# Kernel optimization log

Hardware: AMD Instinct MI355X
Metric: run time of the kernel (lower is better)

Reference implementation:

```python
import jax, jax.numpy as jnp
import numpy as np

B, T, E, H = 2, 2048, 1024, 16
D = E // H
K_KEEP = 391
RECENCY = 64
SCALE = D ** -0.5


def setup_inputs() -> dict:
    key = jax.random.key(0)
    k1, k2, k3 = jax.random.split(key, 3)
    x = jax.random.normal(k1, (B, T, E), jnp.float32)
    W_attn = jax.random.normal(k2, (3 * E, E), jnp.float32) * 0.02  # torch Linear weight [out,in]
    W_proj = jax.random.normal(k3, (E, E), jnp.float32) * 0.02
    return {"x": x, "W_attn": W_attn, "W_proj": W_proj}


def reference(x, W_attn, W_proj):
    b, t, c = x.shape
    qkv = x @ W_attn.T                      # [B,T,3E]
    q, k, v = jnp.split(qkv, 3, axis=-1)
    to_heads = lambda u: u.reshape(b, t, H, D).transpose(0, 2, 1, 3)  # [B,H,T,D]
    q, k, v = to_heads(q), to_heads(k), to_heads(v)

    # first pass: causal attention weights for importance scoring
    scores = jnp.einsum('bhqd,bhkd->bhqk', q, k) * SCALE
    causal = jnp.tril(jnp.ones((t, t), dtype=bool))
    scores = jnp.where(causal, scores, -jnp.inf)
    attn_w = jax.nn.softmax(scores, axis=-1)

    # mean importance over query dim, force-keep recent tokens
    imp = attn_w.mean(axis=2)               # [B,H,T]
    imp = imp.at[:, :, -RECENCY:].set(1.0)

    # top-k token selection per (batch, head)
    _, idx = jax.lax.top_k(imp, K_KEEP)     # [B,H,K]

    # gather pruned K/V
    K_keep = jnp.take_along_axis(k, idx[..., None], axis=2)  # [B,H,K,D]
    V_keep = jnp.take_along_axis(v, idx[..., None], axis=2)

    # second attention pass over pruned keys (no causal mask, matches legacy code)
    s2 = jnp.einsum('bhqd,bhkd->bhqk', q, K_keep) * SCALE
    a2 = jax.nn.softmax(s2, axis=-1)
    out = jnp.einsum('bhqk,bhkd->bhqd', a2, V_keep)          # [B,H,T,D]

    out = out.transpose(0, 2, 1, 3).reshape(b, t, c)
    return out @ W_proj.T
```

## Files before the change

kernel.cpp:

```cpp
#include <hip/hip_runtime.h>
#include <hip/hip_bf16.h>


#define TT 2048
#define EE 1024
#define HH 16
#define DD 64
#define KKEEP 391
#define REC 64
#define NBH 32
#define QSCALE 0.125f
#define KPAD 448

typedef short bf16x8 __attribute__((ext_vector_type(8)));
typedef _Float16 f16x8 __attribute__((ext_vector_type(8)));
typedef float f32x4 __attribute__((ext_vector_type(4)));

#define WAIT_VM(N) asm volatile("s_waitcnt vmcnt(" #N ")" ::: "memory")
#define WAIT_LGKM0 asm volatile("s_waitcnt lgkmcnt(0)" ::: "memory")
#define BAR() __builtin_amdgcn_s_barrier()

static __device__ inline unsigned short bf_rn(float x) {
  unsigned u = __float_as_uint(x);
  unsigned r = u + 0x7fffu + ((u >> 16) & 1u);
  return (unsigned short)(r >> 16);
}
static __device__ inline float bf_up(unsigned short h) {
  return __uint_as_float((unsigned)h << 16);
}
static __device__ inline unsigned pkf16(float a, float b) {
  union { _Float16 h[2]; unsigned u; } t;
  t.h[0] = (_Float16)a; t.h[1] = (_Float16)b; return t.u;
}
static __device__ inline void glds16(const void* g, void* l) {
  __builtin_amdgcn_global_load_lds(
      (const __attribute__((address_space(1))) void*)g,
      (__attribute__((address_space(3))) void*)l, 16, 0, 0);
}

static __device__ inline void split4(const float* __restrict__ src,
                                     unsigned short* __restrict__ ho,
                                     unsigned short* __restrict__ lo_, int i)
{
  float4 v = *reinterpret_cast<const float4*>(&src[i]);
  ushort4 hh, ll;
  float f;
  hh.x = bf_rn(v.x); f = bf_up(hh.x); ll.x = bf_rn(v.x - f);
  hh.y = bf_rn(v.y); f = bf_up(hh.y); ll.y = bf_rn(v.y - f);
  hh.z = bf_rn(v.z); f = bf_up(hh.z); ll.z = bf_rn(v.z - f);
  hh.w = bf_rn(v.w); f = bf_up(hh.w); ll.w = bf_rn(v.w - f);
  *reinterpret_cast<ushort4*>(&ho[i]) = hh;
  *reinterpret_cast<ushort4*>(&lo_[i]) = ll;
}

__global__ __launch_bounds__(256) void split_kernel(
    const float* __restrict__ src, unsigned short* __restrict__ ho,
    unsigned short* __restrict__ lo_, int n)
{
  int i = (blockIdx.x * 256 + threadIdx.x) * 4;
  const int stride = gridDim.x * 1024;
  for (; i < n; i += stride) split4(src, ho, lo_, i);
}

__global__ __launch_bounds__(256) void split2_kernel(
    const float* __restrict__ x, const float* __restrict__ wa,
    unsigned short* __restrict__ xh, unsigned short* __restrict__ xl,
    unsigned short* __restrict__ wh, unsigned short* __restrict__ wl)
{
  const int n1 = 4096 * 1024, n2 = 3072 * 1024;
  int i = (blockIdx.x * 256 + threadIdx.x) * 4;
  const int stride = gridDim.x * 1024;
  for (; i < n1 + n2; i += stride) {
    if (i < n1) split4(x, xh, xl, i);
    else        split4(wa, wh, wl, i - n1);
  }
}

__global__ __launch_bounds__(256) void add_kernel(
    const float* __restrict__ p0, const float* __restrict__ p1,
    float* __restrict__ out, int n)
{
  int i = (blockIdx.x * 256 + threadIdx.x) * 4;
  const int stride = gridDim.x * 1024;
  for (; i < n; i += stride) {
    float4 a = *reinterpret_cast<const float4*>(&p0[i]);
    float4 b = *reinterpret_cast<const float4*>(&p1[i]);
    *reinterpret_cast<float4*>(&out[i]) =
        make_float4(a.x + b.x, a.y + b.y, a.z + b.z, a.w + b.w);
  }
}

template<bool VB, int MODE>
__global__ __launch_bounds__(256) void gemm_pipe(
    const unsigned short* __restrict__ Ah, const unsigned short* __restrict__ Al,
    const unsigned short* __restrict__ Bh, const unsigned short* __restrict__ Bl,
    float* __restrict__ Cc, unsigned short* __restrict__ Qho, unsigned short* __restrict__ Qlo,
    unsigned short* __restrict__ Kho, unsigned short* __restrict__ Klo,
    float* __restrict__ Vo, int M, int N, int Kd, int ldAB, int nOff)
{
  __shared__ __align__(16) unsigned short Ahs[2][128 * 32];
  __shared__ __align__(16) unsigned short Bhs[2][128 * 32];
  __shared__ __align__(16) unsigned short Als[VB ? 1 : 2][128 * 32];
  __shared__ __align__(16) unsigned short Bls[VB ? 1 : 2][128 * 32];
  const int tid = threadIdx.x;
  const int m0 = blockIdx.y * 128, n0 = nOff + blockIdx.x * 128;
  const int kOff = blockIdx.z * Kd;
  const int w = tid >> 6, lane = tid & 63;
  const int wm = w >> 1, wn = w & 1;
  const int l15 = lane & 15, l4 = lane >> 4;

  size_t gA[2], gB[2]; int ldso[2];
#pragma unroll
  for (int s = 0; s < 2; s++) {
    int seg = w * 2 + s;
    int r = seg * 16 + (lane >> 2);
    int kb = (lane & 3) ^ ((r >> 1) & 3);
    gA[s] = (size_t)(m0 + r) * ldAB + kOff + kb * 8;
    gB[s] = (size_t)(n0 + r) * ldAB + kOff + kb * 8;
    ldso[s] = seg * 512;
  }
  auto STAGE = [&](int bb, int k0) {
#pragma unroll
    for (int s = 0; s < 2; s++) {
      glds16(&Ah[gA[s] + k0], &Ahs[bb][ldso[s]]);
      glds16(&Bh[gB[s] + k0], &Bhs[bb][ldso[s]]);
      if (!VB) {
        glds16(&Al[gA[s] + k0], &Als[bb][ldso[s]]);
        glds16(&Bl[gB[s] + k0], &Bls[bb][ldso[s]]);
      }
    }
  };

  f32x4 acc[4][4] = {};

  STAGE(0, 0);
  STAGE(1, 32);
  int cur = 0;
  for (int k0 = 0; k0 < Kd; k0 += 32) {
    if (k0 + 32 < Kd) { if (VB) WAIT_VM(4); else WAIT_VM(8); }
    else WAIT_VM(0);
    BAR();
    bf16x8 ah[4], al[4], bh[4], bl[4];
#pragma unroll
    for (int i = 0; i < 4; i++) {
      int ar = wm * 64 + i * 16 + l15;
      int aoff = ar * 32 + ((l4 ^ ((ar >> 1) & 3)) * 8);
      ah[i] = *reinterpret_cast<const bf16x8*>(&Ahs[cur][aoff]);
      int br = wn * 64 + i * 16 + l15;
      int boff = br * 32 + ((l4 ^ ((br >> 1) & 3)) * 8);
      bh[i] = *reinterpret_cast<const bf16x8*>(&Bhs[cur][boff]);
      if (!VB) {
        al[i] = *reinterpret_cast<const bf16x8*>(&Als[cur][aoff]);
        bl[i] = *reinterpret_cast<const bf16x8*>(&Bls[cur][boff]);
      }
    }
#pragma unroll
    for (int i = 0; i < 4; i++)
#pragma unroll
      for (int j = 0; j < 4; j++) {
        acc[i][j] = __builtin_amdgcn_mfma_f32_16x16x32_bf16(ah[i], bh[j], acc[i][j], 0, 0, 0);
        if (!VB) {
          acc[i][j] = __builtin_amdgcn_mfma_f32_16x16x32_bf16(ah[i], bl[j], acc[i][j], 0, 0, 0);
          acc[i][j] = __builtin_amdgcn_mfma_f32_16x16x32_bf16(al[i], bh[j], acc[i][j], 0, 0, 0);
        }
      }
    WAIT_LGKM0;
    BAR();
    if (k0 + 64 < Kd) STAGE(cur, k0 + 64);
    cur ^= 1;
  }

  if (MODE == 0) {
    float* Cout = Cc + (size_t)blockIdx.z * ((size_t)M * N);
#pragma unroll
    for (int i = 0; i < 4; i++) {
      int mrow0 = m0 + wm * 64 + i * 16 + l4 * 4;
#pragma unroll
      for (int j = 0; j < 4; j++) {
        int ncol = n0 + wn * 64 + j * 16 + l15;
#pragma unroll
        for (int r = 0; r < 4; r++)
          Cout[(size_t)(mrow0 + r) * N + ncol] = acc[i][j][r];
      }
    }
  } else if (VB) {
#pragma unroll
    for (int j = 0; j < 4; j++) {
      int n = n0 + wn * 64 + j * 16 + l15;
      int rr = n & 1023;
      int h = rr >> 6, d0 = rr & 63;
#pragma unroll
      for (int i = 0; i < 4; i++) {
        int mrow0 = m0 + wm * 64 + i * 16 + l4 * 4;
#pragma unroll
        for (int r = 0; r < 4; r++) {
          int m = mrow0 + r;
          int b = m >> 11, t = m & 2047;
          Vo[((size_t)((b * HH + h) * TT + t)) * DD + d0] = acc[i][j][r];
        }
      }
    }
  } else {
#pragma unroll
    for (int j = 0; j < 4; j++) {
      int n = n0 + wn * 64 + j * 16 + l15;
      int p = n >> 10, rr = n & 1023;
      int h = rr >> 6, d0 = rr & 63;
#pragma unroll
      for (int i = 0; i < 4; i++) {
        int mrow0 = m0 + wm * 64 + i * 16 + l4 * 4;
#pragma unroll
        for (int r = 0; r < 4; r++) {
          int m = mrow0 + r;
          int b = m >> 11, t = m & 2047;
          size_t idx = ((size_t)((b * HH + h) * TT + t)) * DD + d0;
          float v = acc[i][j][r];
          unsigned short hi_ = bf_rn(v);
          unsigned short lo2 = bf_rn(v - bf_up(hi_));
          if (p == 0) { Qho[idx] = hi_; Qlo[idx] = lo2; }
          else        { Kho[idx] = hi_; Klo[idx] = lo2; }
        }
      }
    }
  }
}

__global__ __launch_bounds__(512, 4) void importance6_kernel(
    const unsigned short* __restrict__ Qh, const unsigned short* __restrict__ Ql,
    const unsigned short* __restrict__ Kh, const unsigned short* __restrict__ Kl,
    float* __restrict__ part)
{
  const int bh = blockIdx.x;
  const int y = (int)blockIdx.y;
  const int rt = (y < 8) ? (15 - y) : (y - 8);
  const int slab = y;
  const int row0 = rt * 128;
  const int nch = 2 * rt + 2;
  const int tid = threadIdx.x;
  const int w = tid >> 6, lane = tid & 63;
  const int wm = w >> 1, wn = w & 1;
  const int l15 = lane & 15, l4 = lane >> 4;
  __shared__ __align__(16) unsigned short Khs[2][64 * 64];
  __shared__ __align__(16) unsigned short Kls[2][64 * 64];
  __shared__ float csw[8 * 32];
  __shared__ float rsb[2 * 128];

  const int kr = w * 8 + (lane >> 3);
  const int sk8 = (lane & 7) ^ (kr & 7);
  const int ldw = w * 512;
  auto STAGEK1 = [&](int bb, int ci) {
    glds16(&Kh[((size_t)(bh * TT + ci * 64 + kr)) * DD + sk8 * 8], &Khs[bb][ldw]);
  };
  auto STAGEK2 = [&](int bb, int ci) {
    size_t ga = ((size_t)(bh * TT + ci * 64 + kr)) * DD + sk8 * 8;
    glds16(&Kh[ga], &Khs[bb][ldw]);
    glds16(&Kl[ga], &Kls[bb][ldw]);
  };

  bf16x8 aq[2][2];
#pragma unroll
  for (int ks = 0; ks < 2; ks++)
#pragma unroll
    for (int i = 0; i < 2; i++) {
      int ar = wm * 32 + i * 16 + l15;
      size_t ga = ((size_t)(bh * TT + row0 + ar)) * DD + (ks * 4 + l4) * 8;
      aq[ks][i] = *reinterpret_cast<const bf16x8*>(&Qh[ga]);
    }

  float rsum[2][4];
#pragma unroll
  for (int i = 0; i < 2; i++)
#pragma unroll
    for (int r = 0; r < 4; r++) rsum[i][r] = 0.f;

  STAGEK1(0, 0);
  STAGEK1(1, 1);
  int cur = 0;
  for (int ci = 0; ci < nch; ci++) {
    if (ci + 1 < nch) WAIT_VM(1); else WAIT_VM(0);
    BAR();
    f32x4 acc[2][2] = {};
#pragma unroll
    for (int ks = 0; ks < 2; ks++) {
#pragma unroll
      for (int j = 0; j < 2; j++) {
        int br = wn * 32 + j * 16 + l15;
        int off = br * 64 + (((ks * 4 + l4) ^ (br & 7)) * 8);
        bf16x8 bh_ = *reinterpret_cast<const bf16x8*>(&Khs[cur][off]);
#pragma unroll
        for (int i = 0; i < 2; i++)
          acc[i][j] = __builtin_amdgcn_mfma_f32_16x16x32_bf16(aq[ks][i], bh_, acc[i][j], 0, 0, 0);
      }
    }
    if (ci >= 2 * rt) {
#pragma unroll
      for (int i = 0; i < 2; i++)
#pragma unroll
        for (int r = 0; r < 4; r++) {
          int row = row0 + wm * 32 + i * 16 + l4 * 4 + r;
          float s = 0.f;
#pragma unroll
          for (int j = 0; j < 2; j++) {
            int key = ci * 64 + wn * 32 + j * 16 + l15;
            float p = __expf(acc[i][j][r] * QSCALE);
            if (key > row) p = 0.f;
            s += p;
          }
          rsum[i][r] += s;
        }
    } else {
#pragma unroll
      for (int i = 0; i < 2; i++)
#pragma unroll
        for (int r = 0; r < 4; r++) {
          float s = 0.f;
#pragma unroll
          for (int j = 0; j < 2; j++) s += __expf(acc[i][j][r] * QSCALE);
          rsum[i][r] += s;
        }
    }
    WAIT_LGKM0;
    BAR();
    if (ci + 2 < nch) STAGEK1(cur, ci + 2);
    cur ^= 1;
  }
#pragma unroll
  for (int i = 0; i < 2; i++)
#pragma unroll
    for (int r = 0; r < 4; r++) {
      float v = rsum[i][r];
      v += __shfl_xor(v, 1); v += __shfl_xor(v, 2);
      v += __shfl_xor(v, 4); v += __shfl_xor(v, 8);
      rsum[i][r] = v;
    }
  __syncthreads();
  if (l15 == 0) {
#pragma unroll
    for (int i = 0; i < 2; i++)
#pragma unroll
      for (int r = 0; r < 4; r++)
        rsb[wn * 128 + wm * 32 + i * 16 + l4 * 4 + r] = rsum[i][r];
  }
  __syncthreads();
#pragma unroll
  for (int i = 0; i < 2; i++)
#pragma unroll
    for (int r = 0; r < 4; r++) {
      int rl = wm * 32 + i * 16 + l4 * 4 + r;
      rsum[i][r] = 1.0f / (rsb[rl] + rsb[128 + rl]);
    }

  bf16x8 aql[2][2];
#pragma unroll
  for (int ks = 0; ks < 2; ks++)
#pragma unroll
    for (int i = 0; i < 2; i++) {
      int ar = wm * 32 + i * 16 + l15;
      size_t ga = ((size_t)(bh * TT + row0 + ar)) * DD + (ks * 4 + l4) * 8;
      aql[ks][i] = *reinterpret_cast<const bf16x8*>(&Ql[ga]);
    }

  STAGEK2(0, 0);
  STAGEK2(1, 1);
  cur = 0;
  for (int ci = 0; ci < nch; ci++) {
    if (ci + 1 < nch) WAIT_VM(2); else WAIT_VM(0);
    BAR();
    f32x4 acc[2][2] = {};
#pragma unroll
    for (int ks = 0; ks < 2; ks++) {
#pragma unroll
      for (int j = 0; j < 2; j++) {
        int br = wn * 32 + j * 16 + l15;
        int off = br * 64 + (((ks * 4 + l4) ^ (br & 7)) * 8);
        bf16x8 bh_ = *reinterpret_cast<const bf16x8*>(&Khs[cur][off]);
        bf16x8 bl_ = *reinterpret_cast<const bf16x8*>(&Kls[cur][off]);
#pragma unroll
        for (int i = 0; i < 2; i++) {
          acc[i][j] = __builtin_amdgcn_mfma_f32_16x16x32_bf16(aq[ks][i], bh_, acc[i][j], 0, 0, 0);
          acc[i][j] = __builtin_amdgcn_mfma_f32_16x16x32_bf16(aq[ks][i], bl_, acc[i][j], 0, 0, 0);
          acc[i][j] = __builtin_amdgcn_mfma_f32_16x16x32_bf16(aql[ks][i], bh_, acc[i][j], 0, 0, 0);
        }
      }
    }
    float cp[2] = {0.f, 0.f};
    if (ci >= 2 * rt) {
#pragma unroll
      for (int i = 0; i < 2; i++)
#pragma unroll
        for (int r = 0; r < 4; r++) {
          int row = row0 + wm * 32 + i * 16 + l4 * 4 + r;
          float il = rsum[i][r];
#pragma unroll
          for (int j = 0; j < 2; j++) {
            int key = ci * 64 + wn * 32 + j * 16 + l15;
            float p = __expf(acc[i][j][r] * QSCALE) * il;
            if (key > row) p = 0.f;
            cp[j] += p;
          }
        }
    } else {
#pragma unroll
      for (int i = 0; i < 2; i++)
#pragma unroll
        for (int r = 0; r < 4; r++) {
          float il = rsum[i][r];
#pragma unroll
          for (int j = 0; j < 2; j++)
            cp[j] += __expf(acc[i][j][r] * QSCALE) * il;
        }
    }
#pragma unroll
    for (int j = 0; j < 2; j++) {
      float v = cp[j];
      v += __shfl_xor(v, 16); v += __shfl_xor(v, 32);
      cp[j] = v;
    }
    WAIT_LGKM0;
    BAR();
    if (ci + 2 < nch) STAGEK2(cur, ci + 2);
    if (l4 == 0) {
#pragma unroll
      for (int j = 0; j < 2; j++)
        csw[w * 32 + j * 16 + l15] = cp[j];
    }
    WAIT_LGKM0;
    BAR();
    if (tid < 64) {
      int wnc = tid >> 5, cl = tid & 31;
      float s = csw[(0 * 2 + wnc) * 32 + cl] + csw[(1 * 2 + wnc) * 32 + cl] +
                csw[(2 * 2 + wnc) * 32 + cl] + csw[(3 * 2 + wnc) * 32 + cl];
      part[((size_t)(bh * 16 + slab)) * 2048 + ci * 64 + tid] = s;
    }
    cur ^= 1;
  }
}

__global__ __launch_bounds__(256) void topk_gather_kernel(
    const float* __restrict__ part,
    const unsigned short* __restrict__ Kh, const unsigned short* __restrict__ Kl,
    const float* __restrict__ V,
    unsigned short* __restrict__ Kf, unsigned short* __restrict__ Vt)
{
  const int bh = blockIdx.x, tid = threadIdx.x;
  const int lane = tid & 63, w = tid >> 6;
  __shared__ int redi[4];
  __shared__ int stot;
  __shared__ int base[256];
  __shared__ int idxb[KKEEP];
  unsigned u[8];
#pragma unroll
  for (int k = 0; k < 8; k++) {
    int e = tid * 8 + k;
    float s = 0.f;
#pragma unroll
    for (int p = 0; p < 16; p++) {
      int rtp = (p < 8) ? (15 - p) : (p - 8);
      if (e < (rtp + 1) * 128) s += part[((size_t)(bh * 16 + p)) * 2048 + e];
    }
    float v = (e >= TT - REC) ? 3.0e3f : s;
    u[k] = __float_as_uint(v);
  }
  unsigned lo = 0u, hi = 0x7f800000u;
  for (int it = 0; it < 31; it++) {
    unsigned mid = lo + ((hi - lo + 1) >> 1);
    int c = 0;
#pragma unroll
    for (int k = 0; k < 8; k++) c += (u[k] >= mid) ? 1 : 0;
#pragma unroll
    for (int off = 1; off <= 32; off <<= 1) c += __shfl_xor(c, off);
    if (lane == 0) redi[w] = c;
    __syncthreads();
    int tot = redi[0] + redi[1] + redi[2] + redi[3];
    if (tot >= KKEEP) lo = mid; else hi = mid - 1;
    __syncthreads();
  }
  const unsigned vstar = lo;
  int cgt = 0, ceq = 0;
#pragma unroll
  for (int k = 0; k < 8; k++) { cgt += (u[k] > vstar) ? 1 : 0; ceq += (u[k] == vstar) ? 1 : 0; }
  base[tid] = cgt; __syncthreads();
  if (tid == 0) {
    int run = 0;
    for (int i = 0; i < 256; i++) { int t = base[i]; base[i] = run; run += t; }
    stot = run;
  }
  __syncthreads();
  int off1 = base[tid];
#pragma unroll
  for (int k = 0; k < 8; k++)
    if (u[k] > vstar) idxb[off1++] = tid * 8 + k;
  __syncthreads();
  base[tid] = ceq; __syncthreads();
  if (tid == 0) {
    int run = 0;
    for (int i = 0; i < 256; i++) { int t = base[i]; base[i] = run; run += t; }
  }
  __syncthreads();
  int off2 = stot + base[tid];
#pragma unroll
  for (int k = 0; k < 8; k++)
    if (u[k] == vstar) { if (off2 < KKEEP) idxb[off2] = tid * 8 + k; off2++; }
  __syncthreads();
  for (int f = tid; f < KPAD * 8; f += 256) {
    int kk = f >> 3, c8 = f & 7;
    union { _Float16 h[8]; uint4 v; } o;
#pragma unroll
    for (int j = 0; j < 8; j++) o.h[j] = (_Float16)0.f;
    if (kk < KKEEP) {
      int sr = idxb[kk];
      bf16x8 hv = *reinterpret_cast<const bf16x8*>(&Kh[((size_t)(bh * TT + sr)) * DD + c8 * 8]);
      bf16x8 lv = *reinterpret_cast<const bf16x8*>(&Kl[((size_t)(bh * TT + sr)) * DD + c8 * 8]);
#pragma unroll
      for (int j = 0; j < 8; j++)
        o.h[j] = (_Float16)(bf_up((unsigned short)hv[j]) + bf_up((unsigned short)lv[j]));
    }
    *reinterpret_cast<uint4*>(&Kf[((size_t)(bh * KPAD) + kk) * DD + c8 * 8]) = o.v;
  }
  for (int f = tid; f < KPAD * 8; f += 256) {
    int kk = f >> 3, d8 = f & 7;
    float vv[8];
#pragma unroll
    for (int j = 0; j < 8; j++) vv[j] = 0.f;
    if (kk < KKEEP) {
      int sr = idxb[kk];
      float4 a = *reinterpret_cast<const float4*>(&V[((size_t)(bh * TT + sr)) * DD + d8 * 8]);
      float4 b = *reinterpret_cast<const float4*>(&V[((size_t)(bh * TT + sr)) * DD + d8 * 8 + 4]);
      vv[0] = a.x; vv[1] = a.y; vv[2] = a.z; vv[3] = a.w;
      vv[4] = b.x; vv[5] = b.y; vv[6] = b.z; vv[7] = b.w;
    }
#pragma unroll
    for (int j = 0; j < 8; j++) {
      union { _Float16 h; unsigned short s; } t;
      t.h = (_Float16)vv[j];
      Vt[((size_t)(bh * DD) + d8 * 8 + j) * KPAD + kk] = t.s;
    }
  }
}

__global__ __launch_bounds__(256) void attn4_kernel(
    const unsigned short* __restrict__ Qh, const unsigned short* __restrict__ Ql,
    const unsigned short* __restrict__ Kf, const unsigned short* __restrict__ Vt,
    unsigned short* __restrict__ AOh, unsigned short* __restrict__ AOl)
{
  const int rt = blockIdx.y, bh = blockIdx.x;
  const int tid = threadIdx.x;
  const int w = tid >> 6, lane = tid & 63;
  const int l15 = lane & 15, l4 = lane >> 4;
  __shared__ __align__(16) unsigned short Qs[64 * 64];
  __shared__ __align__(16) unsigned short Ks[2][64 * 64];
  __shared__ __align__(16) unsigned short Vs[2][64 * 64];
  __shared__ float LDSo[4][64][16];
  const int row0 = rt * 64;

  int srow[2], skb[2], slds[2];
#pragma unroll
  for (int s = 0; s < 2; s++) {
    int seg = w * 2 + s;
    int r = seg * 8 + (lane >> 3);
    int k8 = lane & 7;
    srow[s] = r; skb[s] = k8 ^ (r & 7); slds[s] = seg * 512;
  }
  auto STAGEA = [&](int bb, int ci) {
#pragma unroll
    for (int s = 0; s < 2; s++) {
      glds16(&Kf[((size_t)(bh * KPAD) + ci * 64 + srow[s]) * DD + skb[s] * 8], &Ks[bb][slds[s]]);
      glds16(&Vt[((size_t)(bh * DD) + srow[s]) * KPAD + ci * 64 + skb[s] * 8], &Vs[bb][slds[s]]);
    }
  };

#pragma unroll
  for (int it = 0; it < 2; it++) {
    int idx = it * 256 + tid;
    int r = idx >> 3, k8 = idx & 7;
    size_t ga = ((size_t)(bh * TT + row0 + r)) * DD + k8 * 8;
    bf16x8 hv = *reinterpret_cast<const bf16x8*>(&Qh[ga]);
    bf16x8 lv = *reinterpret_cast<const bf16x8*>(&Ql[ga]);
    union { _Float16 h[8]; uint4 v; } q16;
#pragma unroll
    for (int j = 0; j < 8; j++)
      q16.h[j] = (_Float16)(bf_up((unsigned short)hv[j]) + bf_up((unsigned short)lv[j]));
    *reinterpret_cast<uint4*>(&Qs[r * 64 + ((k8 ^ (r & 7)) * 8)]) = q16.v;
  }
  STAGEA(0, 0);
  STAGEA(1, 1);
  WAIT_LGKM0;
  BAR();
  f16x8 bq[2];
#pragma unroll
  for (int ks = 0; ks < 2; ks++) {
    int br = w * 16 + l15;
    bq[ks] = *reinterpret_cast<const f16x8*>(&Qs[br * 64 + (((ks * 4 + l4) ^ (br & 7)) * 8)]);
  }

  f32x4 acc_o[4] = {};
  float rsum = 0.f;
  int cur = 0;

  for (int ci = 0; ci < 7; ci++) {
    if (ci + 1 < 7) WAIT_VM(4); else WAIT_VM(0);
    BAR();
    f32x4 accs[4] = {};
#pragma unroll
    for (int ks = 0; ks < 2; ks++) {
#pragma unroll
      for (int i = 0; i < 4; i++) {
        int kr = i * 16 + l15;
        f16x8 af = *reinterpret_cast<const f16x8*>(&Ks[cur][kr * 64 + (((ks * 4 + l4) ^ (kr & 7)) * 8)]);
        accs[i] = __builtin_amdgcn_mfma_f32_16x16x32_f16(af, bq[ks], accs[i], 0, 0, 0);
      }
    }
    float p[4][4];
#pragma unroll
    for (int i = 0; i < 4; i++)
#pragma unroll
      for (int r = 0; r < 4; r++) {
        int gk = ci * 64 + i * 16 + l4 * 4 + r;
        float pp = __expf(accs[i][r] * QSCALE);
        if (gk >= KKEEP) pp = 0.f;
        p[i][r] = pp;
        rsum += pp;
      }
    unsigned pkU[4][2];
#pragma unroll
    for (int i = 0; i < 4; i++) {
      pkU[i][0] = pkf16(p[i][0], p[i][1]);
      pkU[i][1] = pkf16(p[i][2], p[i][3]);
    }
#pragma unroll
    for (int ks = 0; ks < 2; ks++) {
      union { f16x8 h; unsigned u[4]; } bp;
#pragma unroll
      for (int wp = 0; wp < 4; wp++) {
        int src = ((l4 & 1) * 2 + (wp >> 1)) * 16 + l15;
        unsigned v0 = (unsigned)__shfl((int)pkU[ks * 2][wp & 1], src);
        unsigned v1 = (unsigned)__shfl((int)pkU[ks * 2 + 1][wp & 1], src);
        bp.u[wp] = (l4 & 2) ? v1 : v0;
      }
#pragma unroll
      for (int i = 0; i < 4; i++) {
        int dr = i * 16 + l15;
        f16x8 av = *reinterpret_cast<const f16x8*>(&Vs[cur][dr * 64 + (((ks * 4 + l4) ^ (dr & 7)) * 8)]);
        acc_o[i] = __builtin_amdgcn_mfma_f32_16x16x32_f16(av, bp.h, acc_o[i], 0, 0, 0);
      }
    }
    WAIT_LGKM0;
    BAR();
    if (ci + 2 < 7) STAGEA(cur, ci + 2);
    cur ^= 1;
  }
  rsum += __shfl_xor(rsum, 16);
  rsum += __shfl_xor(rsum, 32);
  float inv = 1.0f / rsum;
#pragma unroll
  for (int i = 0; i < 4; i++)
#pragma unroll
    for (int r = 0; r < 4; r++)
      LDSo[w][i * 16 + l4 * 4 + r][l15] = acc_o[i][r] * inv;
  __syncthreads();
  const int b = bh >> 4, h = bh & 15;
#pragma unroll
  for (int uu = 0; uu < 2; uu++) {
    int u = uu * 64 + lane;
    int q = u >> 3, dc = u & 7;
    int row = row0 + w * 16 + q;
    union { unsigned short s[8]; uint4 v; } sh, sl;
#pragma unroll
    for (int j = 0; j < 8; j++) {
      float v = LDSo[w][dc * 8 + j][q];
      unsigned short hh = bf_rn(v);
      sh.s[j] = hh;
      sl.s[j] = bf_rn(v - bf_up(hh));
    }
    size_t addr = ((size_t)(b * TT + row)) * EE + h * DD + dc * 8;
    *reinterpret_cast<uint4*>(&AOh[addr]) = sh.v;
    *reinterpret_cast<uint4*>(&AOl[addr]) = sl.v;
  }
}

extern "C" void kernel_launch(void* const* d_in, const int* in_sizes, int n_in,
                              void* d_out, int out_size, void* d_ws, size_t ws_size,
                              hipStream_t stream)
{
  const float* x     = (const float*)d_in[0];
  const float* Wattn = (const float*)d_in[1];
  const float* Wproj = (const float*)d_in[2];
  float* out = (float*)d_out;
  float* ws  = (float*)d_ws;

  const size_t SZQ = (size_t)NBH * TT * DD;
  const size_t SZK = (size_t)NBH * KPAD * DD;
  float* Vb   = ws;
  float* part = Vb + SZQ;
  unsigned short* Kf  = (unsigned short*)(part + (size_t)NBH * 16 * TT);
  unsigned short* Vt  = Kf + SZK;
  unsigned short* Qhp = Vt + SZK;
  unsigned short* Qlp = Qhp + SZQ;
  unsigned short* Khp = Qlp + SZQ;
  unsigned short* Klp = Khp + SZQ;
  unsigned short* xh  = Klp + SZQ;
  unsigned short* xl  = xh + (size_t)4096 * 1024;
  unsigned short* Wh  = xl + (size_t)4096 * 1024;
  unsigned short* Wl  = Wh + (size_t)3072 * 1024;
  unsigned short* AOh = xh;
  unsigned short* AOl = xl;
  unsigned short* Ph  = Wh;
  unsigned short* Pl  = Ph + (size_t)1024 * 1024;
  float* pb0 = (float*)Qhp;
  float* pb1 = pb0 + SZQ;

  const size_t needB =
      ((size_t)SZQ + (size_t)NBH * 16 * TT) * 4 +
      ((size_t)2 * SZK + (size_t)4 * SZQ + (size_t)2 * 4096 * 1024 + (size_t)2 * 3072 * 1024) * 2;
  if (ws_size < needB) return;

  split2_kernel<<<1024, 256, 0, stream>>>(x, Wattn, xh, xl, Wh, Wl);
  gemm_pipe<false, 1><<<dim3(16, 32), 256, 0, stream>>>(xh, xl, Wh, Wl, nullptr,
      Qhp, Qlp, Khp, Klp, nullptr, 4096, 3072, 1024, 1024, 0);
  gemm_pipe<true, 1><<<dim3(8, 32), 256, 0, stream>>>(xh, xl, Wh, Wl, nullptr,
      nullptr, nullptr, nullptr, nullptr, Vb, 4096, 3072, 1024, 1024, 2048);
  split_kernel<<<256, 256, 0, stream>>>(Wproj, Ph, Pl, 1024 * 1024);
  importance6_kernel<<<dim3(NBH, 16), 512, 0, stream>>>(Qhp, Qlp, Khp, Klp, part);
  topk_gather_kernel<<<NBH, 256, 0, stream>>>(part, Khp, Klp, Vb, Kf, Vt);
  attn4_kernel<<<dim3(NBH, 32), 256, 0, stream>>>(Qhp, Qlp, Kf, Vt, AOh, AOl);
  gemm_pipe<false, 0><<<dim3(8, 32, 2), 256, 0, stream>>>(AOh, AOl, Ph, Pl, pb0,
      nullptr, nullptr, nullptr, nullptr, nullptr, 4096, 1024, 512, 1024, 0);
  add_kernel<<<2048, 256, 0, stream>>>(pb0, pb1, out, 4096 * 1024);
}
```

Before: 265.2 us.

## Split importance kernel into row-sum and column-sum passes over key segments

Replaces the single importance kernel, in which one block per 128-row tile looped over all causal key chunks twice, with two kernels. Each kernel splits the key range into segments of up to 8 chunks, giving 40 blocks per head instead of 16. The first kernel writes partial row sums. The second combines them into inverse normalizers, then computes column contributions per segment. This balances the triangular causal workload and raises parallelism, at the cost of an extra launch, more partial buffers, and a topk reduction over more partials.

```diff
diff --git a/kernel.cpp b/kernel.cpp
--- a/kernel.cpp
+++ b/kernel.cpp
@@ -36,6 +36,13 @@
   __builtin_amdgcn_global_load_lds(
       (const __attribute__((address_space(1))) void*)g,
       (__attribute__((address_space(3))) void*)l, 16, 0, 0);
+}
+
+static __device__ inline void y2rtseg(int y, int& rt, int& seg) {
+  if (y < 4)       { rt = y; seg = 0; }
+  else if (y < 12) { int i = y - 4;  rt = 4 + (i >> 1);  seg = i & 1; }
+  else if (y < 24) { int i = y - 12; rt = 8 + i / 3;     seg = i % 3; }
+  else             { int i = y - 24; rt = 12 + (i >> 2); seg = i & 3; }
 }
 
 static __device__ inline void split4(const float* __restrict__ src,
@@ -225,24 +232,22 @@
   }
 }
 
-__global__ __launch_bounds__(512, 4) void importance6_kernel(
-    const unsigned short* __restrict__ Qh, const unsigned short* __restrict__ Ql,
-    const unsigned short* __restrict__ Kh, const unsigned short* __restrict__ Kl,
-    float* __restrict__ part)
+__global__ __launch_bounds__(512, 4) void imp_rowsum_kernel(
+    const unsigned short* __restrict__ Qh, const unsigned short* __restrict__ Kh,
+    float* __restrict__ rpart)
 {
   const int bh = blockIdx.x;
-  const int y = (int)blockIdx.y;
-  const int rt = (y < 8) ? (15 - y) : (y - 8);
-  const int slab = y;
+  int rt, seg;
+  y2rtseg((int)blockIdx.y, rt, seg);
   const int row0 = rt * 128;
   const int nch = 2 * rt + 2;
+  const int c0 = seg * 8;
+  const int c1 = (c0 + 8 < nch) ? (c0 + 8) : nch;
   const int tid = threadIdx.x;
   const int w = tid >> 6, lane = tid & 63;
   const int wm = w >> 1, wn = w & 1;
   const int l15 = lane & 15, l4 = lane >> 4;
   __shared__ __align__(16) unsigned short Khs[2][64 * 64];
-  __shared__ __align__(16) unsigned short Kls[2][64 * 64];
-  __shared__ float csw[8 * 32];
   __shared__ float rsb[2 * 128];
 
   const int kr = w * 8 + (lane >> 3);
@@ -251,11 +256,6 @@
   auto STAGEK1 = [&](int bb, int ci) {
     glds16(&Kh[((size_t)(bh * TT + ci * 64 + kr)) * DD + sk8 * 8], &Khs[bb][ldw]);
   };
-  auto STAGEK2 = [&](int bb, int ci) {
-    size_t ga = ((size_t)(bh * TT + ci * 64 + kr)) * DD + sk8 * 8;
-    glds16(&Kh[ga], &Khs[bb][ldw]);
-    glds16(&Kl[ga], &Kls[bb][ldw]);
-  };
 
   bf16x8 aq[2][2];
 #pragma unroll
@@ -273,11 +273,11 @@
 #pragma unroll
     for (int r = 0; r < 4; r++) rsum[i][r] = 0.f;
 
-  STAGEK1(0, 0);
-  STAGEK1(1, 1);
+  STAGEK1(0, c0);
+  if (c0 + 1 < c1) STAGEK1(1, c0 + 1);
   int cur = 0;
-  for (int ci = 0; ci < nch; ci++) {
-    if (ci + 1 < nch) WAIT_VM(1); else WAIT_VM(0);
+  for (int ci = c0; ci < c1; ci++) {
+    if (ci + 1 < c1) WAIT_VM(1); else WAIT_VM(0);
     BAR();
     f32x4 acc[2][2] = {};
 #pragma unroll
@@ -321,7 +321,7 @@
     }
     WAIT_LGKM0;
     BAR();
-    if (ci + 2 < nch) STAGEK1(cur, ci + 2);
+    if (ci + 2 < c1) STAGEK1(cur, ci + 2);
     cur ^= 1;
   }
 #pragma unroll
@@ -342,29 +342,70 @@
         rsb[wn * 128 + wm * 32 + i * 16 + l4 * 4 + r] = rsum[i][r];
   }
   __syncthreads();
+  if (tid < 128)
+    rpart[(((size_t)(bh * 16 + rt)) * 4 + seg) * 128 + tid] = rsb[tid] + rsb[128 + tid];
+}
+
+__global__ __launch_bounds__(512, 4) void imp_colsum_kernel(
+    const unsigned short* __restrict__ Qh, const unsigned short* __restrict__ Ql,
+    const unsigned short* __restrict__ Kh, const unsigned short* __restrict__ Kl,
+    const float* __restrict__ rpart, float* __restrict__ partc)
+{
+  const int bh = blockIdx.x;
+  const int y = (int)blockIdx.y;
+  int rt, seg;
+  y2rtseg(y, rt, seg);
+  const int row0 = rt * 128;
+  const int nch = 2 * rt + 2;
+  const int nseg = (2 * rt + 9) >> 3;
+  const int c0 = seg * 8;
+  const int c1 = (c0 + 8 < nch) ? (c0 + 8) : nch;
+  const int tid = threadIdx.x;
+  const int w = tid >> 6, lane = tid & 63;
+  const int wm = w >> 1, wn = w & 1;
+  const int l15 = lane & 15, l4 = lane >> 4;
+  __shared__ __align__(16) unsigned short Khs[2][64 * 64];
+  __shared__ __align__(16) unsigned short Kls[2][64 * 64];
+  __shared__ float csw[8 * 32];
+
+  const int kr = w * 8 + (lane >> 3);
+  const int sk8 = (lane & 7) ^ (kr & 7);
+  const int ldw = w * 512;
+  auto STAGEK2 = [&](int bb, int ci) {
+    size_t ga = ((size_t)(bh * TT + ci * 64 + kr)) * DD + sk8 * 8;
+    glds16(&Kh[ga], &Khs[bb][ldw]);
+    glds16(&Kl[ga], &Kls[bb][ldw]);
+  };
+
+  STAGEK2(0, c0);
+  if (c0 + 1 < c1) STAGEK2(1, c0 + 1);
+
+  float invl[2][4];
 #pragma unroll
   for (int i = 0; i < 2; i++)
 #pragma unroll
     for (int r = 0; r < 4; r++) {
-      int rl = wm * 32 + i * 16 + l4 * 4 + r;
-      rsum[i][r] = 1.0f / (rsb[rl] + rsb[128 + rl]);
-    }
-
-  bf16x8 aql[2][2];
+      int rowLocal = wm * 32 + i * 16 + l4 * 4 + r;
+      float s = 0.f;
+      for (int sg = 0; sg < nseg; sg++)
+        s += rpart[(((size_t)(bh * 16 + rt)) * 4 + sg) * 128 + rowLocal];
+      invl[i][r] = 1.0f / s;
+    }
+
+  bf16x8 aq[2][2], aql[2][2];
 #pragma unroll
   for (int ks = 0; ks < 2; ks++)
 #pragma unroll
     for (int i = 0; i < 2; i++) {
       int ar = wm * 32 + i * 16 + l15;
       size_t ga = ((size_t)(bh * TT + row0 + ar)) * DD + (ks * 4 + l4) * 8;
+      aq[ks][i]  = *reinterpret_cast<const bf16x8*>(&Qh[ga]);
       aql[ks][i] = *reinterpret_cast<const bf16x8*>(&Ql[ga]);
     }
 
-  STAGEK2(0, 0);
-  STAGEK2(1, 1);
-  cur = 0;
-  for (int ci = 0; ci < nch; ci++) {
-    if (ci + 1 < nch) WAIT_VM(2); else WAIT_VM(0);
+  int cur = 0;
+  for (int ci = c0; ci < c1; ci++) {
+    if (ci + 1 < c1) WAIT_VM(2); else WAIT_VM(0);
     BAR();
     f32x4 acc[2][2] = {};
 #pragma unroll
@@ -390,7 +431,7 @@
 #pragma unroll
         for (int r = 0; r < 4; r++) {
           int row = row0 + wm * 32 + i * 16 + l4 * 4 + r;
-          float il = rsum[i][r];
+          float il = invl[i][r];
 #pragma unroll
           for (int j = 0; j < 2; j++) {
             int key = ci * 64 + wn * 32 + j * 16 + l15;
@@ -404,7 +445,7 @@
       for (int i = 0; i < 2; i++)
 #pragma unroll
         for (int r = 0; r < 4; r++) {
-          float il = rsum[i][r];
+          float il = invl[i][r];
 #pragma unroll
           for (int j = 0; j < 2; j++)
             cp[j] += __expf(acc[i][j][r] * QSCALE) * il;
@@ -418,7 +459,7 @@
     }
     WAIT_LGKM0;
     BAR();
-    if (ci + 2 < nch) STAGEK2(cur, ci + 2);
+    if (ci + 2 < c1) STAGEK2(cur, ci + 2);
     if (l4 == 0) {
 #pragma unroll
       for (int j = 0; j < 2; j++)
@@ -430,14 +471,14 @@
       int wnc = tid >> 5, cl = tid & 31;
       float s = csw[(0 * 2 + wnc) * 32 + cl] + csw[(1 * 2 + wnc) * 32 + cl] +
                 csw[(2 * 2 + wnc) * 32 + cl] + csw[(3 * 2 + wnc) * 32 + cl];
-      part[((size_t)(bh * 16 + slab)) * 2048 + ci * 64 + tid] = s;
+      partc[((size_t)(bh * 40 + y)) * 512 + (ci - c0) * 64 + tid] = s;
     }
     cur ^= 1;
   }
 }
 
 __global__ __launch_bounds__(256) void topk_gather_kernel(
-    const float* __restrict__ part,
+    const float* __restrict__ partc,
     const unsigned short* __restrict__ Kh, const unsigned short* __restrict__ Kl,
     const float* __restrict__ V,
     unsigned short* __restrict__ Kf, unsigned short* __restrict__ Vt)
@@ -453,10 +494,11 @@
   for (int k = 0; k < 8; k++) {
     int e = tid * 8 + k;
     float s = 0.f;
-#pragma unroll
-    for (int p = 0; p < 16; p++) {
-      int rtp = (p < 8) ? (15 - p) : (p - 8);
-      if (e < (rtp + 1) * 128) s += part[((size_t)(bh * 16 + p)) * 2048 + e];
+    for (int rt = e >> 7; rt < 16; rt++) {
+      int yb = (rt < 4) ? rt : (rt < 8) ? 4 + 2 * (rt - 4)
+             : (rt < 12) ? 12 + 3 * (rt - 8) : 24 + 4 * (rt - 12);
+      yb += (e >> 9);
+      s += partc[((size_t)(bh * 40 + yb)) * 512 + (e & 511)];
     }
     float v = (e >= TT - REC) ? 3.0e3f : s;
     u[k] = __float_as_uint(v);
@@ -690,9 +732,10 @@
 
   const size_t SZQ = (size_t)NBH * TT * DD;
   const size_t SZK = (size_t)NBH * KPAD * DD;
-  float* Vb   = ws;
-  float* part = Vb + SZQ;
-  unsigned short* Kf  = (unsigned short*)(part + (size_t)NBH * 16 * TT);
+  float* Vb    = ws;
+  float* rpart = Vb + SZQ;
+  float* partc = rpart + (size_t)NBH * 16 * 4 * 128;
+  unsigned short* Kf  = (unsigned short*)(rpart + (size_t)NBH * 16 * TT);
   unsigned short* Vt  = Kf + SZK;
   unsigned short* Qhp = Vt + SZK;
   unsigned short* Qlp = Qhp + SZQ;
@@ -720,8 +763,9 @@
   gemm_pipe<true, 1><<<dim3(8, 32), 256, 0, stream>>>(xh, xl, Wh, Wl, nullptr,
       nullptr, nullptr, nullptr, nullptr, Vb, 4096, 3072, 1024, 1024, 2048);
   split_kernel<<<256, 256, 0, stream>>>(Wproj, Ph, Pl, 1024 * 1024);
-  importance6_kernel<<<dim3(NBH, 16), 512, 0, stream>>>(Qhp, Qlp, Khp, Klp, part);
-  topk_gather_kernel<<<NBH, 256, 0, stream>>>(part, Khp, Klp, Vb, Kf, Vt);
+  imp_rowsum_kernel<<<dim3(NBH, 40), 512, 0, stream>>>(Qhp, Khp, rpart);
+  imp_colsum_kernel<<<dim3(NBH, 40), 512, 0, stream>>>(Qhp, Qlp, Khp, Klp, rpart, partc);
+  topk_gather_kernel<<<NBH, 256, 0, stream>>>(partc, Khp, Klp, Vb, Kf, Vt);
   attn4_kernel<<<dim3(NBH, 32), 256, 0, stream>>>(Qhp, Qlp, Kf, Vt, AOh, AOl);
   gemm_pipe<false, 0><<<dim3(8, 32, 2), 256, 0, stream>>>(AOh, AOl, Ph, Pl, pb0,
       nullptr, nullptr, nullptr, nullptr, nullptr, 4096, 1024, 512, 1024, 0);
```

Result: slower. 284.7 us (+7.4%).
